# Kernel optimization log

Hardware: AMD Instinct MI355X
Metric: run time of the kernel (lower is better)

The kernel has to match this reference:

```python
import jax, jax.numpy as jnp
import numpy as np

N_TYPES = 5
TEMPERATURE = 1.0
CLIP = 0.3
PADDING_INDEX = -1


def setup_inputs() -> dict:
    key = jax.random.key(0)
    k1, k2, k3 = jax.random.split(key, 3)
    B, A, P = 8, 128, 8192
    coords = jax.random.normal(k1, (B, A, 3), dtype=jnp.float32)
    atom_types = jax.random.randint(k2, (B, A), 0, N_TYPES)
    query_points = jax.random.normal(k3, (B, P, 3), dtype=jnp.float32)
    return {"coords": coords, "atom_types": atom_types, "query_points": query_points}


def reference(coords, atom_types, query_points):
    # coords: [B,A,3], atom_types: [B,A] int, query_points: [B,P,3]
    # diff[b,p,a] = coords[b,a] - query_points[b,p]  (atom - query, matches torch coords_exp - q_exp)
    diff = coords[:, None, :, :] - query_points[:, :, None, :]      # [B,P,A,3]
    dist = jnp.sqrt(jnp.sum(diff * diff, axis=-1))                   # [B,P,A]

    valid = atom_types != PADDING_INDEX                              # [B,A]
    type_mask = (atom_types[..., None] == jnp.arange(N_TYPES)) & valid[..., None]  # [B,A,T]
    mask = type_mask[:, None, :, :]                                  # [B,1,A,T]

    logits = (-dist / TEMPERATURE)[..., None]                        # [B,P,A,1]
    neg = jnp.where(mask, logits, -jnp.inf)                          # [B,P,A,T]
    m = jnp.max(neg, axis=2, keepdims=True)                          # [B,P,1,T]
    m_safe = jnp.where(jnp.isfinite(m), m, 0.0)
    e = jnp.where(mask, jnp.exp(neg - m_safe), 0.0)                  # [B,P,A,T]
    denom = jnp.sum(e, axis=2, keepdims=True)                        # [B,P,1,T]
    w = e / jnp.where(denom > 0, denom, 1.0)                         # masked softmax over atoms

    # weighted sum of diffs per atom type -> [B,P,T,3]
    grads = jnp.einsum('bpat,bpad->bptd', w, diff)

    # gradient magnitude clipping
    mag = jnp.sqrt(jnp.sum(grads * grads, axis=-1, keepdims=True))   # [B,P,T,1]
    clip_mask = mag > CLIP
    safe_mag = jnp.where(clip_mask, mag, 1.0)
    grads = jnp.where(clip_mask, grads * (CLIP / safe_mag), grads)
    return grads  # [B,P,T,3]
```

## Files before the change

### kernel.cpp

```cpp
#include <hip/hip_runtime.h>


#define B_DIM 8
#define A_DIM 128
#define P_DIM 8192
#define N_TYPES 5
#define KSPLIT 4
#define PTS_PER_BLOCK 64

__global__ __launch_bounds__(256) void gnf_kernel(
    const float* __restrict__ coords,
    const int*   __restrict__ atom_types,
    const float* __restrict__ query,
    float*       __restrict__ out)
{
    __shared__ float4 s_atoms[A_DIM];
    __shared__ int s_cnt[N_TYPES];
    __shared__ int s_seg[N_TYPES + 1];
    __shared__ int s_cur[N_TYPES];

    const int blocks_per_b = P_DIM / PTS_PER_BLOCK;
    const int b  = blockIdx.x / blocks_per_b;
    const int p0 = (blockIdx.x % blocks_per_b) * PTS_PER_BLOCK;
    const int tid = threadIdx.x;

    if (tid < N_TYPES) s_cnt[tid] = 0;
    __syncthreads();

    float ax = 0.f, ay = 0.f, az = 0.f;
    int ty = -1;
    if (tid < A_DIM) {
        const float* c = coords + (size_t)(b * A_DIM + tid) * 3;
        ax = c[0]; ay = c[1]; az = c[2];
        int t = atom_types[b * A_DIM + tid];
        if (t >= 0 && t < N_TYPES) {
            ty = t;
            atomicAdd(&s_cnt[t], 1);
        }
    }
    __syncthreads();
    if (tid == 0) {
        int run = 0;
#pragma unroll
        for (int t = 0; t < N_TYPES; ++t) {
            s_seg[t] = run; s_cur[t] = run; run += s_cnt[t];
        }
        s_seg[N_TYPES] = run;
    }
    __syncthreads();
    if (ty >= 0) {
        int pos = atomicAdd(&s_cur[ty], 1);
        s_atoms[pos] = make_float4(ax, ay, az, 0.f);
    }
    __syncthreads();

    int seg[N_TYPES + 1];
#pragma unroll
    for (int t = 0; t <= N_TYPES; ++t) seg[t] = s_seg[t];

    const int k = tid & (KSPLIT - 1);
    const int p = p0 + (tid >> 2);
    const float* q = query + (size_t)(b * P_DIM + p) * 3;
    const float qx = q[0], qy = q[1], qz = q[2];
    float* o = out + (size_t)(b * P_DIM + p) * (N_TYPES * 3);

#pragma unroll
    for (int t = 0; t < N_TYPES; ++t) {
        float s = 0.f, gx = 0.f, gy = 0.f, gz = 0.f;
        for (int i = seg[t] + k; i < seg[t + 1]; i += KSPLIT) {
            const float4 at = s_atoms[i];
            const float dx = at.x - qx;
            const float dy = at.y - qy;
            const float dz = at.z - qz;
            const float d2 = fmaf(dx, dx, fmaf(dy, dy, dz * dz));
            const float dist = sqrtf(d2);
            const float e = __builtin_exp2f(dist * -1.44269504088896340736f);
            s += e;
            gx = fmaf(e, dx, gx);
            gy = fmaf(e, dy, gy);
            gz = fmaf(e, dz, gz);
        }
        s  += __shfl_xor(s, 1);  s  += __shfl_xor(s, 2);
        gx += __shfl_xor(gx, 1); gx += __shfl_xor(gx, 2);
        gy += __shfl_xor(gy, 1); gy += __shfl_xor(gy, 2);
        gz += __shfl_xor(gz, 1); gz += __shfl_xor(gz, 2);

        const float inv = (s > 0.f) ? (1.0f / s) : 0.0f;
        float x = gx * inv, y = gy * inv, z = gz * inv;
        const float mag = sqrtf(fmaf(x, x, fmaf(y, y, z * z)));
        if (mag > 0.3f) {
            const float sc = 0.3f / mag;
            x *= sc; y *= sc; z *= sc;
        }
        const float val = (k == 0) ? x : ((k == 1) ? y : z);
        if (k < 3) o[t * 3 + k] = val;
    }
}

extern "C" void kernel_launch(void* const* d_in, const int* in_sizes, int n_in,
                              void* d_out, int out_size, void* d_ws, size_t ws_size,
                              hipStream_t stream) {
    const float* coords     = (const float*)d_in[0];
    const int*   atom_types = (const int*)d_in[1];
    const float* query      = (const float*)d_in[2];
    float*       out        = (float*)d_out;

    const int nblocks = (B_DIM * P_DIM * KSPLIT) / 256;
    gnf_kernel<<<nblocks, 256, 0, stream>>>(coords, atom_types, query, out);
}
```

Baseline: 17.36 us.

## Split atoms over 8 lanes per point and use fast AMDGCN math intrinsics

Raises the atom split per query point from 4 to 8 lanes, halving points per block and doubling the block count. The point's query load moves ahead of the shared-memory setup so its latency overlaps the atom sort. sqrt and exp2 become raw AMDGCN intrinsics, and the per-type normalize and clip use rcp and rsq. Each type's result is now kept by one lane and written once at the end, which replaces the per-type scattered stores. This adds a third shuffle round per reduction and per-block setup cost, and the approximate intrinsics lose some precision.

```diff
diff --git a/kernel.cpp b/kernel.cpp
--- a/kernel.cpp
+++ b/kernel.cpp
@@ -4,9 +4,9 @@
 #define B_DIM 8
 #define A_DIM 128
 #define P_DIM 8192
-#define N_TYPES 5
-#define KSPLIT 4
-#define PTS_PER_BLOCK 64
+#define NT 5
+#define KSPLIT 8
+#define PTS_PER_BLOCK 32
 
 __global__ __launch_bounds__(256) void gnf_kernel(
     const float* __restrict__ coords,
@@ -15,16 +15,21 @@
     float*       __restrict__ out)
 {
     __shared__ float4 s_atoms[A_DIM];
-    __shared__ int s_cnt[N_TYPES];
-    __shared__ int s_seg[N_TYPES + 1];
-    __shared__ int s_cur[N_TYPES];
+    __shared__ int s_cnt[NT];
+    __shared__ int s_seg[NT + 1];
+    __shared__ int s_cur[NT];
 
-    const int blocks_per_b = P_DIM / PTS_PER_BLOCK;
-    const int b  = blockIdx.x / blocks_per_b;
-    const int p0 = (blockIdx.x % blocks_per_b) * PTS_PER_BLOCK;
     const int tid = threadIdx.x;
+    const int b   = blockIdx.x >> 8;
+    const int p0  = (blockIdx.x & 255) * PTS_PER_BLOCK;
 
-    if (tid < N_TYPES) s_cnt[tid] = 0;
+    const int k = tid & (KSPLIT - 1);
+    const int p = p0 + (tid >> 3);
+
+    const float* q = query + (size_t)(b * P_DIM + p) * 3;
+    const float qx = q[0], qy = q[1], qz = q[2];
+
+    if (tid < NT) s_cnt[tid] = 0;
     __syncthreads();
 
     float ax = 0.f, ay = 0.f, az = 0.f;
@@ -33,19 +38,14 @@
         const float* c = coords + (size_t)(b * A_DIM + tid) * 3;
         ax = c[0]; ay = c[1]; az = c[2];
         int t = atom_types[b * A_DIM + tid];
-        if (t >= 0 && t < N_TYPES) {
-            ty = t;
-            atomicAdd(&s_cnt[t], 1);
-        }
+        if (t >= 0 && t < NT) { ty = t; atomicAdd(&s_cnt[t], 1); }
     }
     __syncthreads();
     if (tid == 0) {
         int run = 0;
 #pragma unroll
-        for (int t = 0; t < N_TYPES; ++t) {
-            s_seg[t] = run; s_cur[t] = run; run += s_cnt[t];
-        }
-        s_seg[N_TYPES] = run;
+        for (int t = 0; t < NT; ++t) { s_seg[t] = run; s_cur[t] = run; run += s_cnt[t]; }
+        s_seg[NT] = run;
     }
     __syncthreads();
     if (ty >= 0) {
@@ -54,18 +54,13 @@
     }
     __syncthreads();
 
-    int seg[N_TYPES + 1];
+    int seg[NT + 1];
 #pragma unroll
-    for (int t = 0; t <= N_TYPES; ++t) seg[t] = s_seg[t];
+    for (int t = 0; t <= NT; ++t) seg[t] = s_seg[t];
 
-    const int k = tid & (KSPLIT - 1);
-    const int p = p0 + (tid >> 2);
-    const float* q = query + (size_t)(b * P_DIM + p) * 3;
-    const float qx = q[0], qy = q[1], qz = q[2];
-    float* o = out + (size_t)(b * P_DIM + p) * (N_TYPES * 3);
-
+    float ox = 0.f, oy = 0.f, oz = 0.f;
 #pragma unroll
-    for (int t = 0; t < N_TYPES; ++t) {
+    for (int t = 0; t < NT; ++t) {
         float s = 0.f, gx = 0.f, gy = 0.f, gz = 0.f;
         for (int i = seg[t] + k; i < seg[t + 1]; i += KSPLIT) {
             const float4 at = s_atoms[i];
@@ -73,27 +68,33 @@
             const float dy = at.y - qy;
             const float dz = at.z - qz;
             const float d2 = fmaf(dx, dx, fmaf(dy, dy, dz * dz));
-            const float dist = sqrtf(d2);
-            const float e = __builtin_exp2f(dist * -1.44269504088896340736f);
+            const float e  = __builtin_amdgcn_exp2f(
+                __builtin_amdgcn_sqrtf(d2) * -1.44269504088896340736f);
             s += e;
             gx = fmaf(e, dx, gx);
             gy = fmaf(e, dy, gy);
             gz = fmaf(e, dz, gz);
         }
-        s  += __shfl_xor(s, 1);  s  += __shfl_xor(s, 2);
-        gx += __shfl_xor(gx, 1); gx += __shfl_xor(gx, 2);
-        gy += __shfl_xor(gy, 1); gy += __shfl_xor(gy, 2);
-        gz += __shfl_xor(gz, 1); gz += __shfl_xor(gz, 2);
+        s  += __shfl_xor(s, 1);  s  += __shfl_xor(s, 2);  s  += __shfl_xor(s, 4);
+        gx += __shfl_xor(gx, 1); gx += __shfl_xor(gx, 2); gx += __shfl_xor(gx, 4);
+        gy += __shfl_xor(gy, 1); gy += __shfl_xor(gy, 2); gy += __shfl_xor(gy, 4);
+        gz += __shfl_xor(gz, 1); gz += __shfl_xor(gz, 2); gz += __shfl_xor(gz, 4);
 
-        const float inv = (s > 0.f) ? (1.0f / s) : 0.0f;
-        float x = gx * inv, y = gy * inv, z = gz * inv;
-        const float mag = sqrtf(fmaf(x, x, fmaf(y, y, z * z)));
-        if (mag > 0.3f) {
-            const float sc = 0.3f / mag;
-            x *= sc; y *= sc; z *= sc;
+        if (k == t) {
+            const float inv = (s > 0.f) ? __builtin_amdgcn_rcpf(s) : 0.0f;
+            float x = gx * inv, y = gy * inv, z = gz * inv;
+            const float m2 = fmaf(x, x, fmaf(y, y, z * z));
+            if (m2 > 0.09f) {
+                const float sc = 0.3f * __builtin_amdgcn_rsqf(m2);
+                x *= sc; y *= sc; z *= sc;
+            }
+            ox = x; oy = y; oz = z;
         }
-        const float val = (k == 0) ? x : ((k == 1) ? y : z);
-        if (k < 3) o[t * 3 + k] = val;
+    }
+
+    if (k < NT) {
+        float* o = out + (size_t)(b * P_DIM + p) * (NT * 3) + k * 3;
+        o[0] = ox; o[1] = oy; o[2] = oz;
     }
 }
 
@@ -105,6 +106,6 @@
     const float* query      = (const float*)d_in[2];
     float*       out        = (float*)d_out;
 
-    const int nblocks = (B_DIM * P_DIM * KSPLIT) / 256;
+    const int nblocks = (B_DIM * P_DIM) / PTS_PER_BLOCK;
     gnf_kernel<<<nblocks, 256, 0, stream>>>(coords, atom_types, query, out);
 }
```

Result: faster. 15.55 us (-10.4%).
